# Optimization experiments

Hardware: AMD Instinct MI355X
Metric: run time of the kernel (lower is better)

Reference implementation:

```python
import jax, jax.numpy as jnp
import numpy as np

B, T, N = 1024, 1024, 32


def setup_inputs() -> dict:
    key = jax.random.key(0)
    k1, k2, k3 = jax.random.split(key, 3)
    logits = jax.random.normal(k1, (B, T, N), dtype=jnp.float32)
    transitions = jax.random.normal(k2, (N, N), dtype=jnp.float32) * 0.1
    sequence_lengths = jax.random.randint(k3, (B,), 0, T, dtype=jnp.int32)
    return {"logits": logits, "transitions": transitions, "sequence_lengths": sequence_lengths}


def reference(logits, transitions, sequence_lengths):
    # Viterbi decode (tfa.text.crf.crf_decode), then mask padding positions to 0.
    Bd, Td, Nd = logits.shape
    tag_ids = jnp.arange(Nd, dtype=jnp.int32)
    init_state = logits[:, 0, :]  # [B, N] viterbi scores at t=0

    def step(state, xs):
        logit_t, t = xs
        # scores[b, prev, cur] = state[b, prev] + transitions[prev, cur]
        scores = state[:, :, None] + transitions[None, :, :]  # [B, N, N]
        bp = jnp.argmax(scores, axis=1).astype(jnp.int32)      # [B, N] best prev tag
        new_state = jnp.max(scores, axis=1) + logit_t          # [B, N]
        valid = (t < sequence_lengths)[:, None]                # step t valid if t <= len-1
        state = jnp.where(valid, new_state, state)             # freeze state past seq end
        bp = jnp.where(valid, bp, tag_ids[None, :])            # identity backptr past end
        return state, bp

    xs = (jnp.swapaxes(logits[:, 1:, :], 0, 1), jnp.arange(1, Td))
    final_state, bps = jax.lax.scan(step, init_state, xs)      # bps: [T-1, B, N]
    last_tag = jnp.argmax(final_state, axis=-1).astype(jnp.int32)  # [B]

    def back(tag, bp):
        prev = jnp.take_along_axis(bp, tag[:, None], axis=1)[:, 0]
        return prev, tag  # emit tag at position i+1, carry tag at position i

    first_tag, later = jax.lax.scan(back, last_tag, bps, reverse=True)
    pred = jnp.concatenate([first_tag[:, None], jnp.swapaxes(later, 0, 1)], axis=1)  # [B, T]
    mask = (jnp.arange(Td)[None, :] < sequence_lengths[:, None]).astype(pred.dtype)
    return pred * mask
```

## Files before the change

### kernel.cpp

```cpp
#include <hip/hip_runtime.h>
#include <stdint.h>

#define T_LEN 1024
#define NSTATE 32

__device__ __forceinline__ float max3f(float a, float b, float c) {
    return fmaxf(fmaxf(a, b), c);
}

__launch_bounds__(64)
__global__ void viterbi_kernel(const float* __restrict__ logits,
                               const float* __restrict__ trans,
                               const int* __restrict__ seqlen,
                               int* __restrict__ out)
{
    const int lane = threadIdx.x;
    const int j    = lane & 31;

    __shared__ uint8_t bp[T_LEN * NSTATE];
    __shared__ uint8_t Farr[32 * 32];
    __shared__ uint8_t earr[32];
    __shared__ __align__(16) int pred[T_LEN];

    int L = seqlen[blockIdx.x];
    if (L < 0) L = 0;
    if (L > 1023) L = 1023;

    float tr[NSTATE];
#pragma unroll
    for (int k = 0; k < NSTATE; ++k)
        tr[k] = trans[k * NSTATE + j];

    const float* lg = logits + (size_t)blockIdx.x * T_LEN * NSTATE;

    float ns = lg[j];

    auto step = [&](int t, float lgt) {
        int nsb = __float_as_int(ns);
        float v[NSTATE];
#pragma unroll
        for (int k = 0; k < NSTATE; ++k) {
            int sk = __builtin_amdgcn_readlane(nsb, k);
            v[k] = __int_as_float(sk) + tr[k];
        }

        float g0 = max3f(v[0],  v[1],  v[2]);
        float g1 = max3f(v[3],  v[4],  v[5]);
        float g2 = max3f(v[6],  v[7],  v[8]);
        float g3 = max3f(v[9],  v[10], v[11]);
        float g4 = max3f(v[12], v[13], v[14]);
        float g5 = max3f(v[15], v[16], v[17]);
        float g6 = max3f(v[18], v[19], v[20]);
        float g7 = max3f(v[21], v[22], v[23]);
        float g8 = max3f(v[24], v[25], v[26]);
        float g9 = max3f(v[27], v[28], v[29]);
        float g10 = fmaxf(v[30], v[31]);
        float h0 = max3f(g0, g1, g2);
        float h1 = max3f(g3, g4, g5);
        float h2 = max3f(g6, g7, g8);
        float h3 = fmaxf(g9, g10);
        float gm = fmaxf(max3f(h0, h1, h2), h3);

        ns = gm + lgt;

        int ia = 64, ib = 64;
#pragma unroll
        for (int k = 15; k >= 0; --k) ia = (v[k] == gm) ? k : ia;
#pragma unroll
        for (int k = 31; k >= 16; --k) ib = (v[k] == gm) ? k : ib;
        int idx = min(ia, ib);

        bp[t * NSTATE + j] = (uint8_t)idx;
    };

    if (L >= 2) {
        float pre[8];
#pragma unroll
        for (int d = 0; d < 8; ++d) {
            int tp = 1 + d; if (tp > 1023) tp = 1023;
            pre[d] = lg[tp * NSTATE + j];
        }
        int t = 1;
        for (; t + 8 <= L; t += 8) {
#pragma unroll
            for (int u = 0; u < 8; ++u) {
                step(t + u, pre[u]);
                int tp = t + 8 + u; if (tp > 1023) tp = 1023;
                pre[u] = lg[tp * NSTATE + j];
            }
        }
        for (int k = 0; t < L; ++t, ++k) step(t, pre[k]);
    }

    float m = ns;
#pragma unroll
    for (int d = 1; d < 32; d <<= 1) m = fmaxf(m, __shfl_xor(m, d));
    int ii = (ns == m) ? j : 64;
#pragma unroll
    for (int d = 1; d < 32; d <<= 1) ii = min(ii, __shfl_xor(ii, d));
    const int ft = ii;

    __syncthreads();

    if (L >= 2) {
        const int c = lane & 31;
        const int j0base = (lane >> 5) * 16;
        int tags[16];
#pragma unroll
        for (int k = 0; k < 16; ++k) tags[k] = j0base + k;
        const int thi = c * 32 + 31;
        for (int s = 0; s < 32; ++s) {
            int t = thi - s;
            bool valid = (t >= 1) && (t <= L - 1);
            int tc = t < 1 ? 1 : (t > L - 1 ? L - 1 : t);
            int base = tc * NSTATE;
#pragma unroll
            for (int k = 0; k < 16; ++k) {
                int nt = bp[base + tags[k]];
                tags[k] = valid ? nt : tags[k];
            }
        }
#pragma unroll
        for (int k = 0; k < 16; ++k)
            Farr[c * 32 + j0base + k] = (uint8_t)tags[k];
        __syncthreads();

        if (lane == 0) {
            int e = ft;
            for (int c2 = 31; c2 >= 0; --c2) {
                earr[c2] = (uint8_t)e;
                e = Farr[c2 * 32 + e];
            }
        }
        __syncthreads();

        if (lane < 32) {
            int tag = earr[lane];
            const int thi3 = lane * 32 + 31;
            for (int s = 0; s < 32; ++s) {
                int t = thi3 - s;
                pred[t] = (t < L) ? tag : 0;
                bool valid = (t >= 1) && (t <= L - 1);
                int tc = t < 1 ? 1 : (t > L - 1 ? L - 1 : t);
                int nt = bp[tc * NSTATE + tag];
                tag = valid ? nt : tag;
            }
        }
        __syncthreads();
    } else {
#pragma unroll
        for (int r = 0; r < 16; ++r) pred[lane * 16 + r] = 0;
        __syncthreads();
        if (lane == 0 && L == 1) pred[0] = ft;
        __syncthreads();
    }

    int4* out4 = reinterpret_cast<int4*>(out + (size_t)blockIdx.x * T_LEN);
    const int4* p4 = reinterpret_cast<const int4*>(pred);
#pragma unroll
    for (int r = 0; r < 4; ++r)
        out4[r * 64 + lane] = p4[r * 64 + lane];
}

extern "C" void kernel_launch(void* const* d_in, const int* in_sizes, int n_in,
                              void* d_out, int out_size, void* d_ws, size_t ws_size,
                              hipStream_t stream) {
    const float* logits = (const float*)d_in[0];
    const float* trans  = (const float*)d_in[1];
    const int*   slen   = (const int*)d_in[2];
    int*         out    = (int*)d_out;
    const int B = in_sizes[2];

    viterbi_kernel<<<dim3(B), dim3(64), 0, stream>>>(logits, trans, slen, out);
}
```

Before: 289.4 us.

## Pack two sequences per wavefront and broadcast state through LDS vector loads

Each 64-lane wave now decodes two batch elements, one per 32-lane half, so the number of blocks is halved and the otherwise idle upper half-wave does useful work. Because readlane cannot broadcast separately within each half, the per-step state is written to shared memory and read back with eight float4 loads. The backtrace is restructured so each half handles its own sequence with 32 tags per lane. The cost is a serial loop that runs to the longer of the two lengths, extra LDS round-trips on the recurrence's critical path, and doubled shared memory per block.

```diff
diff --git a/kernel.cpp b/kernel.cpp
--- a/kernel.cpp
+++ b/kernel.cpp
@@ -15,34 +15,54 @@
                                int* __restrict__ out)
 {
     const int lane = threadIdx.x;
+    const int half = lane >> 5;
     const int j    = lane & 31;
 
-    __shared__ uint8_t bp[T_LEN * NSTATE];
-    __shared__ uint8_t Farr[32 * 32];
-    __shared__ uint8_t earr[32];
-    __shared__ __align__(16) int pred[T_LEN];
+    __shared__ __align__(16) float st[2][NSTATE];
+    __shared__ uint8_t bp[2][T_LEN * NSTATE];
+    __shared__ uint8_t Farr[2][NSTATE * NSTATE];
+    __shared__ uint8_t earr[2][NSTATE];
+    __shared__ __align__(16) int pred[2][T_LEN];
 
-    int L = seqlen[blockIdx.x];
-    if (L < 0) L = 0;
-    if (L > 1023) L = 1023;
+    const int bid = blockIdx.x;
+    int LA = seqlen[2 * bid], LB = seqlen[2 * bid + 1];
+    LA = min(max(LA, 0), T_LEN);
+    LB = min(max(LB, 0), T_LEN);
+    const int Lm   = half ? LB : LA;
+    const int maxL = max(LA, LB);
 
     float tr[NSTATE];
 #pragma unroll
     for (int k = 0; k < NSTATE; ++k)
         tr[k] = trans[k * NSTATE + j];
 
-    const float* lg = logits + (size_t)blockIdx.x * T_LEN * NSTATE;
+    const float* lg = logits + (size_t)(2 * bid + half) * T_LEN * NSTATE;
 
     float ns = lg[j];
 
+    const float4* stv = reinterpret_cast<const float4*>(st[half]);
+    uint8_t* bph = bp[half];
+
     auto step = [&](int t, float lgt) {
-        int nsb = __float_as_int(ns);
+        st[half][j] = ns;
+        float4 q0 = stv[0];
+        float4 q1 = stv[1];
+        float4 q2 = stv[2];
+        float4 q3 = stv[3];
+        float4 q4 = stv[4];
+        float4 q5 = stv[5];
+        float4 q6 = stv[6];
+        float4 q7 = stv[7];
+
         float v[NSTATE];
-#pragma unroll
-        for (int k = 0; k < NSTATE; ++k) {
-            int sk = __builtin_amdgcn_readlane(nsb, k);
-            v[k] = __int_as_float(sk) + tr[k];
-        }
+        v[0]=q0.x+tr[0];  v[1]=q0.y+tr[1];  v[2]=q0.z+tr[2];  v[3]=q0.w+tr[3];
+        v[4]=q1.x+tr[4];  v[5]=q1.y+tr[5];  v[6]=q1.z+tr[6];  v[7]=q1.w+tr[7];
+        v[8]=q2.x+tr[8];  v[9]=q2.y+tr[9];  v[10]=q2.z+tr[10];v[11]=q2.w+tr[11];
+        v[12]=q3.x+tr[12];v[13]=q3.y+tr[13];v[14]=q3.z+tr[14];v[15]=q3.w+tr[15];
+        v[16]=q4.x+tr[16];v[17]=q4.y+tr[17];v[18]=q4.z+tr[18];v[19]=q4.w+tr[19];
+        v[20]=q5.x+tr[20];v[21]=q5.y+tr[21];v[22]=q5.z+tr[22];v[23]=q5.w+tr[23];
+        v[24]=q6.x+tr[24];v[25]=q6.y+tr[25];v[26]=q6.z+tr[26];v[27]=q6.w+tr[27];
+        v[28]=q7.x+tr[28];v[29]=q7.y+tr[29];v[30]=q7.z+tr[30];v[31]=q7.w+tr[31];
 
         float g0 = max3f(v[0],  v[1],  v[2]);
         float g1 = max3f(v[3],  v[4],  v[5]);
@@ -61,7 +81,8 @@
         float h3 = fmaxf(g9, g10);
         float gm = fmaxf(max3f(h0, h1, h2), h3);
 
-        ns = gm + lgt;
+        const bool act = t < Lm;
+        ns = act ? gm + lgt : ns;
 
         int ia = 64, ib = 64;
 #pragma unroll
@@ -70,10 +91,10 @@
         for (int k = 31; k >= 16; --k) ib = (v[k] == gm) ? k : ib;
         int idx = min(ia, ib);
 
-        bp[t * NSTATE + j] = (uint8_t)idx;
+        if (act) bph[t * NSTATE + j] = (uint8_t)idx;
     };
 
-    if (L >= 2) {
+    if (maxL >= 2) {
         float pre[8];
 #pragma unroll
         for (int d = 0; d < 8; ++d) {
@@ -81,7 +102,7 @@
             pre[d] = lg[tp * NSTATE + j];
         }
         int t = 1;
-        for (; t + 8 <= L; t += 8) {
+        for (; t + 8 <= maxL; t += 8) {
 #pragma unroll
             for (int u = 0; u < 8; ++u) {
                 step(t + u, pre[u]);
@@ -89,7 +110,7 @@
                 pre[u] = lg[tp * NSTATE + j];
             }
         }
-        for (int k = 0; t < L; ++t, ++k) step(t, pre[k]);
+        for (int k = 0; t < maxL; ++t, ++k) step(t, pre[k]);
     }
 
     float m = ns;
@@ -102,64 +123,56 @@
 
     __syncthreads();
 
-    if (L >= 2) {
-        const int c = lane & 31;
-        const int j0base = (lane >> 5) * 16;
-        int tags[16];
+    {
+        int tags[NSTATE];
 #pragma unroll
-        for (int k = 0; k < 16; ++k) tags[k] = j0base + k;
-        const int thi = c * 32 + 31;
+        for (int k = 0; k < NSTATE; ++k) tags[k] = k;
+        const int thi = j * 32 + 31;
         for (int s = 0; s < 32; ++s) {
             int t = thi - s;
-            bool valid = (t >= 1) && (t <= L - 1);
-            int tc = t < 1 ? 1 : (t > L - 1 ? L - 1 : t);
+            bool valid = (t >= 1) && (t <= Lm - 1);
+            int tc = min(max(t, 1), max(Lm - 1, 1));
             int base = tc * NSTATE;
 #pragma unroll
-            for (int k = 0; k < 16; ++k) {
-                int nt = bp[base + tags[k]];
+            for (int k = 0; k < NSTATE; ++k) {
+                int nt = bph[base + tags[k]];
                 tags[k] = valid ? nt : tags[k];
             }
         }
 #pragma unroll
-        for (int k = 0; k < 16; ++k)
-            Farr[c * 32 + j0base + k] = (uint8_t)tags[k];
-        __syncthreads();
+        for (int k = 0; k < NSTATE; ++k)
+            Farr[half][j * NSTATE + k] = (uint8_t)tags[k];
+    }
+    __syncthreads();
 
-        if (lane == 0) {
-            int e = ft;
-            for (int c2 = 31; c2 >= 0; --c2) {
-                earr[c2] = (uint8_t)e;
-                e = Farr[c2 * 32 + e];
-            }
+    if (j == 0) {
+        int e = ft;
+        for (int c2 = 31; c2 >= 0; --c2) {
+            earr[half][c2] = (uint8_t)e;
+            e = Farr[half][c2 * NSTATE + e];
         }
-        __syncthreads();
+    }
+    __syncthreads();
 
-        if (lane < 32) {
-            int tag = earr[lane];
-            const int thi3 = lane * 32 + 31;
-            for (int s = 0; s < 32; ++s) {
-                int t = thi3 - s;
-                pred[t] = (t < L) ? tag : 0;
-                bool valid = (t >= 1) && (t <= L - 1);
-                int tc = t < 1 ? 1 : (t > L - 1 ? L - 1 : t);
-                int nt = bp[tc * NSTATE + tag];
-                tag = valid ? nt : tag;
-            }
+    {
+        int tag = earr[half][j];
+        const int thi3 = j * 32 + 31;
+        for (int s = 0; s < 32; ++s) {
+            int t = thi3 - s;
+            pred[half][t] = (t < Lm) ? tag : 0;
+            bool valid = (t >= 1) && (t <= Lm - 1);
+            int tc = min(max(t, 1), max(Lm - 1, 1));
+            int nt = bph[tc * NSTATE + tag];
+            tag = valid ? nt : tag;
         }
-        __syncthreads();
-    } else {
+    }
+    __syncthreads();
+
+    int4* o4 = reinterpret_cast<int4*>(out + (size_t)(2 * bid + half) * T_LEN);
+    const int4* p4 = reinterpret_cast<const int4*>(pred[half]);
 #pragma unroll
-        for (int r = 0; r < 16; ++r) pred[lane * 16 + r] = 0;
-        __syncthreads();
-        if (lane == 0 && L == 1) pred[0] = ft;
-        __syncthreads();
-    }
-
-    int4* out4 = reinterpret_cast<int4*>(out + (size_t)blockIdx.x * T_LEN);
-    const int4* p4 = reinterpret_cast<const int4*>(pred);
-#pragma unroll
-    for (int r = 0; r < 4; ++r)
-        out4[r * 64 + lane] = p4[r * 64 + lane];
+    for (int r = 0; r < 8; ++r)
+        o4[r * 32 + j] = p4[r * 32 + j];
 }
 
 extern "C" void kernel_launch(void* const* d_in, const int* in_sizes, int n_in,
@@ -171,5 +184,5 @@
     int*         out    = (int*)d_out;
     const int B = in_sizes[2];
 
-    viterbi_kernel<<<dim3(B), dim3(64), 0, stream>>>(logits, trans, slen, out);
+    viterbi_kernel<<<dim3(B / 2), dim3(64), 0, stream>>>(logits, trans, slen, out);
 }
```

Result: slower. 438.2 us (+51.4%).
